# Kernel tuning notes

Hardware: AMD Instinct MI355X
Metric: run time of the kernel (lower is better)

## Reference

```python
import jax, jax.numpy as jnp
import numpy as np

CUTOFF = 5.0
N_GAUSS = 25
LOG2 = 0.6931471805599453
N_INTER = 3


def ssp(x):
    # shifted softplus used by SchNet
    return jax.nn.softplus(x) - LOG2


def setup_inputs() -> dict:
    key = jax.random.key(0)
    ks = jax.random.split(key, 16)
    B, A, N, F, G, Z = 16, 128, 127, 128, N_GAUSS, 100
    s = 1.0 / np.sqrt(F)
    emb = jax.random.normal(ks[0], (Z, F), jnp.float32)
    emb = emb.at[0].set(0.0)  # padding_idx=0
    inp = {
        "positions": jax.random.normal(ks[1], (B, A, 3), jnp.float32) * 3.0,
        "cell": jnp.zeros((B, 3, 3), jnp.float32),
        "cell_offset": jnp.zeros((B, A, N, 3), jnp.float32),
        "neighbor_mask": jnp.ones((B, A, N), jnp.float32),
        "embeddings": emb,
        "filt_W1": jax.random.normal(ks[2], (N_INTER, G, F), jnp.float32) / np.sqrt(G),
        "filt_b1": jnp.zeros((N_INTER, F), jnp.float32),
        "filt_W2": jax.random.normal(ks[3], (N_INTER, F, F), jnp.float32) * s,
        "filt_b2": jnp.zeros((N_INTER, F), jnp.float32),
        "in2f_W": jax.random.normal(ks[4], (N_INTER, F, F), jnp.float32) * s,
        "f2out_W": jax.random.normal(ks[5], (N_INTER, F, F), jnp.float32) * s,
        "f2out_b": jnp.zeros((N_INTER, F), jnp.float32),
        "dense_W": jax.random.normal(ks[6], (N_INTER, F, F), jnp.float32) * s,
        "dense_b": jnp.zeros((N_INTER, F), jnp.float32),
        "atomic_numbers": jax.random.randint(ks[7], (B, A), 1, Z).astype(jnp.int32),
        "neighbors": jax.random.randint(ks[8], (B, A, N), 0, A).astype(jnp.int32),
    }
    return inp


def _schnet_forward(positions, cell, cell_offset, neighbor_mask, embeddings,
                    filt_W1, filt_b1, filt_W2, filt_b2,
                    in2f_W, f2out_W, f2out_b, dense_W, dense_b,
                    atomic_numbers, neighbors):
    B, A, _ = positions.shape
    bidx = jnp.arange(B)[:, None, None]

    # ---- AtomDistances: gather neighbor positions, pairwise distances ----
    pos_nbh = positions[bidx, neighbors]            # [B,A,N,3]
    dvec = pos_nbh - positions[:, :, None, :]
    dvec = dvec + jnp.einsum('banj,bjc->banc', cell_offset, cell)
    d2 = jnp.sum(dvec * dvec, axis=-1)              # [B,A,N]
    m = neighbor_mask > 0
    r_ij = jnp.where(m, jnp.sqrt(jnp.where(m, d2, 1.0)), 0.0)

    # ---- GaussianSmearing(0, cutoff, 25) ----
    centers = jnp.linspace(0.0, CUTOFF, N_GAUSS, dtype=r_ij.dtype)
    width = centers[1] - centers[0]
    coeff = -0.5 / (width * width)
    diff = r_ij[..., None] - centers                # [B,A,N,G]
    f_ij = jnp.exp(coeff * diff * diff)

    # ---- CosineCutoff ----
    C = 0.5 * (jnp.cos(r_ij * jnp.pi / CUTOFF) + 1.0)
    C = C * (r_ij < CUTOFF).astype(r_ij.dtype)      # [B,A,N]

    # ---- embedding ----
    x = embeddings[atomic_numbers]                  # [B,A,F]

    # ---- interaction blocks (cfconv + dense residual) ----
    for l in range(N_INTER):
        W = ssp(jnp.einsum('bang,gf->banf', f_ij, filt_W1[l]) + filt_b1[l])
        W = jnp.einsum('banf,fg->bang', W, filt_W2[l]) + filt_b2[l]
        W = W * C[..., None]                        # [B,A,N,F]
        y = x @ in2f_W[l]                           # [B,A,F], no bias
        y_nbh = y[bidx, neighbors]                  # [B,A,N,F]
        agg = jnp.sum(y_nbh * W * neighbor_mask[..., None], axis=2)  # [B,A,F]
        v = ssp(agg @ f2out_W[l] + f2out_b[l])
        v = v @ dense_W[l] + dense_b[l]
        x = x + v
    return x


def reference(positions, cell, cell_offset, neighbor_mask, embeddings,
              filt_W1, filt_b1, filt_W2, filt_b2,
              in2f_W, f2out_W, f2out_b, dense_W, dense_b,
              atomic_numbers, neighbors):
    return _schnet_forward(positions, cell, cell_offset, neighbor_mask, embeddings,
                           filt_W1, filt_b1, filt_W2, filt_b2,
                           in2f_W, f2out_W, f2out_b, dense_W, dense_b,
                           atomic_numbers, neighbors)
```

## Files before the change

### kernel.cpp

```cpp
#include <hip/hip_runtime.h>
#include <math.h>

#define BB 16
#define AA 128
#define NNB 127
#define FF 128
#define GG 25

typedef __attribute__((ext_vector_type(8))) short bf16x8;
typedef __attribute__((ext_vector_type(4))) float f32x4;
typedef unsigned short ushort_t;

#define GLOBAL_LOAD_LDS16(gp, lp)                                                        \
    __builtin_amdgcn_global_load_lds((const __attribute__((address_space(1))) unsigned int*)(gp), \
                                     (__attribute__((address_space(3))) unsigned int*)(lp), 16, 0, 0)

__device__ __forceinline__ float ssp_f(float x) {
    return fmaxf(x, 0.f) + log1pf(__expf(-fabsf(x))) - 0.6931471805599453f;
}

__device__ __forceinline__ float ssp_fast(float x) {
    float e = __expf(-fabsf(x));
    float p = fmaf(e, 0.03215845f, -0.13606275f);
    p = fmaf(e, p, 0.28947478f);
    p = fmaf(e, p, -0.49190896f);
    p = fmaf(e, p, 0.99949556f);
    return fmaxf(x, 0.f) + e * p - 0.6931471805599453f;
}

__device__ __forceinline__ ushort_t f2bf(float f) {
    unsigned int u = __float_as_uint(f);
    unsigned int r = (u + 0x7fffu + ((u >> 16) & 1u)) >> 16;
    return (ushort_t)r;
}

__device__ __forceinline__ float bf2f(ushort_t h) {
    return __uint_as_float(((unsigned int)h) << 16);
}

__device__ __forceinline__ unsigned int pack2bf(float lo, float hi) {
    return (unsigned int)f2bf(lo) | ((unsigned int)f2bf(hi) << 16);
}

__global__ __launch_bounds__(256) void k_prep(const float* __restrict__ W1,
                                              const float* __restrict__ W2,
                                              const float* __restrict__ Win,
                                              const float* __restrict__ Wf,
                                              const float* __restrict__ Wd,
                                              ushort_t* __restrict__ w1t,
                                              ushort_t* __restrict__ w2s,
                                              ushort_t* __restrict__ whi,
                                              ushort_t* __restrict__ wlo) {
    int i = blockIdx.x * 256 + threadIdx.x;
    if (i < 3 * 128 * 32) {
        int l = i >> 12, rem = i & 4095, f = rem >> 5, g = rem & 31;
        float v = (g < GG) ? W1[l * GG * FF + g * FF + f] : 0.f;
        w1t[i] = f2bf(v);
    }
    if (i < 3 * 16384) {
        int l = i >> 14, rem = i & 16383, f = rem >> 7, k = rem & 127;
        w2s[l * 16384 + f * 128 + (k ^ ((f & 7) << 3))] = f2bf(W2[l * 16384 + k * FF + f]);
    }
    if (i < 9 * 16384) {
        int m = i / 49152;
        int rem = i - m * 49152;
        int l = rem >> 14;
        int rk = rem & 16383;
        int f = rk >> 7, k = rk & 127;
        const float* src = (m == 0) ? Win : ((m == 1) ? Wf : Wd);
        float v = src[l * 16384 + k * 128 + f];
        ushort_t h = f2bf(v);
        whi[i] = h;
        wlo[i] = f2bf(v - bf2f(h));
    }
}

__global__ __launch_bounds__(256) void k_init_x(const float* __restrict__ emb,
                                                const int* __restrict__ z,
                                                float* __restrict__ x) {
    int i = blockIdx.x * 256 + threadIdx.x;
    if (i < BB * AA * FF) {
        int row = i >> 7, f = i & 127;
        x[i] = emb[z[row] * FF + f];
    }
}

__global__ __launch_bounds__(512) void k_ffn(
    const float* __restrict__ agg, const float* __restrict__ x_in,
    float* __restrict__ x_out, float* __restrict__ y, float* __restrict__ out,
    const ushort_t* __restrict__ wfh, const ushort_t* __restrict__ wfl, const float* __restrict__ bfv_g,
    const ushort_t* __restrict__ wdh, const ushort_t* __restrict__ wdl, const float* __restrict__ bdv_g,
    const ushort_t* __restrict__ wih, const ushort_t* __restrict__ wil,
    int mode) {
    __shared__ ushort_t tsh[8][136];
    __shared__ ushort_t tsl[8][136];
    const int t = threadIdx.x;
    const int lane = t & 63, w = t >> 6;
    const int l15 = lane & 15, l4 = lane >> 4;
    const int r0 = blockIdx.x << 3;
    const int fcol = (w << 4) + l15;

    bf16x8 Ah[4], Al[4];

    auto loadA_global = [&](const float* __restrict__ M) {
#pragma unroll
        for (int ks = 0; ks < 4; ++ks) {
            float v[8];
            if (l15 < 8) {
                const float4* p = (const float4*)(M + ((size_t)(r0 + l15) << 7) + (ks << 5) + (l4 << 3));
                float4 a = p[0], b = p[1];
                v[0] = a.x; v[1] = a.y; v[2] = a.z; v[3] = a.w;
                v[4] = b.x; v[5] = b.y; v[6] = b.z; v[7] = b.w;
            } else {
#pragma unroll
                for (int j = 0; j < 8; ++j) v[j] = 0.f;
            }
#pragma unroll
            for (int j = 0; j < 8; ++j) {
                ushort_t h = f2bf(v[j]);
                Ah[ks][j] = (short)h;
                Al[ks][j] = (short)f2bf(v[j] - bf2f(h));
            }
        }
    };
    auto loadA_lds = [&]() {
#pragma unroll
        for (int ks = 0; ks < 4; ++ks) {
            if (l15 < 8) {
                const char* base = (const char*)&tsh[l15][0] + (ks << 6) + (l4 << 4);
                Ah[ks] = *(const bf16x8*)base;
                const char* basel = (const char*)&tsl[l15][0] + (ks << 6) + (l4 << 4);
                Al[ks] = *(const bf16x8*)basel;
            } else {
#pragma unroll
                for (int j = 0; j < 8; ++j) { Ah[ks][j] = 0; Al[ks][j] = 0; }
            }
        }
    };

    if (mode & 1) {
        loadA_global(agg);
        float bfv = bfv_g[fcol];
        f32x4 acc = {bfv, bfv, bfv, bfv};
#pragma unroll
        for (int ks = 0; ks < 4; ++ks) {
            const bf16x8 Bh = *(const bf16x8*)(wfh + ((size_t)fcol << 7) + (ks << 5) + (l4 << 3));
            const bf16x8 Bl = *(const bf16x8*)(wfl + ((size_t)fcol << 7) + (ks << 5) + (l4 << 3));
            acc = __builtin_amdgcn_mfma_f32_16x16x32_bf16(Al[ks], Bh, acc, 0, 0, 0);
            acc = __builtin_amdgcn_mfma_f32_16x16x32_bf16(Ah[ks], Bl, acc, 0, 0, 0);
            acc = __builtin_amdgcn_mfma_f32_16x16x32_bf16(Ah[ks], Bh, acc, 0, 0, 0);
        }
#pragma unroll
        for (int reg = 0; reg < 4; ++reg) {
            int r = (l4 << 2) + reg;
            if (r < 8) {
                float v = ssp_f(acc[reg]);
                ushort_t h = f2bf(v);
                tsh[r][fcol] = h;
                tsl[r][fcol] = f2bf(v - bf2f(h));
            }
        }
        __syncthreads();
        loadA_lds();
        float bdv = bdv_g[fcol];
        f32x4 acc2 = {bdv, bdv, bdv, bdv};
#pragma unroll
        for (int ks = 0; ks < 4; ++ks) {
            const bf16x8 Bh = *(const bf16x8*)(wdh + ((size_t)fcol << 7) + (ks << 5) + (l4 << 3));
            const bf16x8 Bl = *(const bf16x8*)(wdl + ((size_t)fcol << 7) + (ks << 5) + (l4 << 3));
            acc2 = __builtin_amdgcn_mfma_f32_16x16x32_bf16(Al[ks], Bh, acc2, 0, 0, 0);
            acc2 = __builtin_amdgcn_mfma_f32_16x16x32_bf16(Ah[ks], Bl, acc2, 0, 0, 0);
            acc2 = __builtin_amdgcn_mfma_f32_16x16x32_bf16(Ah[ks], Bh, acc2, 0, 0, 0);
        }
        __syncthreads();
#pragma unroll
        for (int reg = 0; reg < 4; ++reg) {
            int r = (l4 << 2) + reg;
            if (r < 8) {
                size_t gi = ((size_t)(r0 + r) << 7) + fcol;
                float xn = x_in[gi] + acc2[reg];
                x_out[gi] = xn;
                if (mode & 4) out[gi] = xn;
                if (mode & 2) {
                    ushort_t h = f2bf(xn);
                    tsh[r][fcol] = h;
                    tsl[r][fcol] = f2bf(xn - bf2f(h));
                }
            }
        }
        if (mode & 2) __syncthreads();
    }
    if (mode & 2) {
        if (mode & 1) loadA_lds(); else loadA_global(x_in);
        f32x4 acc3 = {0.f, 0.f, 0.f, 0.f};
#pragma unroll
        for (int ks = 0; ks < 4; ++ks) {
            const bf16x8 Bh = *(const bf16x8*)(wih + ((size_t)fcol << 7) + (ks << 5) + (l4 << 3));
            const bf16x8 Bl = *(const bf16x8*)(wil + ((size_t)fcol << 7) + (ks << 5) + (l4 << 3));
            acc3 = __builtin_amdgcn_mfma_f32_16x16x32_bf16(Al[ks], Bh, acc3, 0, 0, 0);
            acc3 = __builtin_amdgcn_mfma_f32_16x16x32_bf16(Ah[ks], Bl, acc3, 0, 0, 0);
            acc3 = __builtin_amdgcn_mfma_f32_16x16x32_bf16(Ah[ks], Bh, acc3, 0, 0, 0);
        }
#pragma unroll
        for (int reg = 0; reg < 4; ++reg) {
            int r = (l4 << 2) + reg;
            if (r < 8) y[((size_t)(r0 + r) << 7) + fcol] = acc3[reg];
        }
    }
}

#define SMEM_BYTES 67072

__global__ __launch_bounds__(512, 4) void k_cfconv(
    const float* __restrict__ positions, const float* __restrict__ cell,
    const float* __restrict__ cell_offset, const float* __restrict__ nmask,
    const int* __restrict__ neighbors,
    const ushort_t* __restrict__ w1t, const float* __restrict__ b1,
    const ushort_t* __restrict__ w2s, const float* __restrict__ b2,
    const float* __restrict__ y, float* __restrict__ agg) {
    extern __shared__ char smem[];
    float* cm_s = (float*)(smem + 65536);
    int* nbr_s = (int*)(smem + 66048);
    float* r_s = (float*)(smem + 66560);
    float* y_s = (float*)smem;
    float* red_s = (float*)smem;

    const int row = blockIdx.x;
    const int b = row >> 7;
    const int t = threadIdx.x;
    const int lane = t & 63, w = t >> 6;
    const int l15 = lane & 15, l4 = lane >> 4;

    {
        const char* gsrc = (const char*)w2s;
#pragma unroll
        for (int i = 0; i < 4; ++i) {
            int blk = (w << 2) + i;
            GLOBAL_LOAD_LDS16(gsrc + (blk << 10) + (lane << 4), smem + 32768 + (blk << 10));
        }
    }

    if (t < NNB) {
        int nb = neighbors[row * NNB + t];
        nbr_s[t] = nb;
        float px = positions[row * 3 + 0], py = positions[row * 3 + 1], pz = positions[row * 3 + 2];
        int nrow = b * AA + nb;
        float qx = positions[nrow * 3 + 0], qy = positions[nrow * 3 + 1], qz = positions[nrow * 3 + 2];
        const float* co = cell_offset + (size_t)row * NNB * 3 + (size_t)t * 3;
        const float* cl = cell + b * 9;
        float c0 = co[0], c1 = co[1], c2 = co[2];
        float ox = c0 * cl[0] + c1 * cl[3] + c2 * cl[6];
        float oy = c0 * cl[1] + c1 * cl[4] + c2 * cl[7];
        float oz = c0 * cl[2] + c1 * cl[5] + c2 * cl[8];
        float dx = qx - px + ox, dy = qy - py + oy, dz = qz - pz + oz;
        float d2 = dx * dx + dy * dy + dz * dz;
        float mk = nmask[row * NNB + t];
        float r = (mk > 0.f) ? sqrtf(d2) : 0.f;
        r_s[t] = r;
        float Cc = 0.5f * (__cosf(r * (3.14159265358979323846f / 5.0f)) + 1.f);
        Cc = (r < 5.0f) ? Cc : 0.f;
        cm_s[t] = Cc * mk;
    } else if (t == NNB) {
        cm_s[NNB] = 0.f; nbr_s[NNB] = 0; r_s[NNB] = 1e9f;
    }
    __syncthreads();

    {
        const int nrow = (w << 4) + l15;
        const float rv = r_s[nrow];
        const float width = 5.0f / (GG - 1);
        const float coeff = -0.5f / (width * width);
        bf16x8 fb;
#pragma unroll
        for (int j = 0; j < 8; ++j) {
            int g = (l4 << 3) + j;
            float d = rv - g * width;
            float v = (g < GG && nrow < NNB) ? __expf(coeff * d * d) : 0.f;
            fb[j] = (short)f2bf(v);
        }
        const int base = nrow * 256;
        const int sw = (nrow & 7) << 4;
#pragma unroll
        for (int ft = 0; ft < 8; ++ft) {
            bf16x8 aw = *(const bf16x8*)(w1t + ((ft << 4) + l15) * 32 + (l4 << 3));
            const int f0 = (ft << 4) + (l4 << 2);
            f32x4 c0 = *(const f32x4*)(b1 + f0);
            f32x4 d = __builtin_amdgcn_mfma_f32_16x16x32_bf16(aw, fb, c0, 0, 0, 0);
            unsigned long long pk =
                (unsigned long long)pack2bf(ssp_fast(d[0]), ssp_fast(d[1])) |
                ((unsigned long long)pack2bf(ssp_fast(d[2]), ssp_fast(d[3])) << 32);
            *(unsigned long long*)(smem + base + ((f0 << 1) ^ sw)) = pk;
        }
    }
    __syncthreads();

    const int wr = w >> 2, wc = w & 3;
    f32x4 acc[4][2];
#pragma unroll
    for (int mi = 0; mi < 4; ++mi)
#pragma unroll
        for (int ft = 0; ft < 2; ++ft) {
            float b2v = b2[(wc << 5) + (ft << 4) + l15];
            f32x4 c0 = {b2v, b2v, b2v, b2v};
            acc[mi][ft] = c0;
        }
#pragma unroll
    for (int ks = 0; ks < 4; ++ks) {
        bf16x8 ha[4];
#pragma unroll
        for (int mi = 0; mi < 4; ++mi) {
            int n = (wr << 6) + (mi << 4) + l15;
            ha[mi] = *(const bf16x8*)(smem + n * 256 + ((((ks << 2) + l4) << 4) ^ ((n & 7) << 4)));
        }
        bf16x8 wbv[2];
#pragma unroll
        for (int ft = 0; ft < 2; ++ft) {
            int f = (wc << 5) + (ft << 4) + l15;
            wbv[ft] = *(const bf16x8*)(smem + 32768 + f * 256 + ((((ks << 2) + l4) << 4) ^ ((f & 7) << 4)));
        }
#pragma unroll
        for (int mi = 0; mi < 4; ++mi) {
            acc[mi][0] = __builtin_amdgcn_mfma_f32_16x16x32_bf16(ha[mi], wbv[0], acc[mi][0], 0, 0, 0);
            acc[mi][1] = __builtin_amdgcn_mfma_f32_16x16x32_bf16(ha[mi], wbv[1], acc[mi][1], 0, 0, 0);
        }
    }
    __syncthreads();

    {
        const int bA = b * AA;
#pragma unroll
        for (int ii = 0; ii < 8; ++ii) {
            int c = t + (ii << 9);
            int n = c >> 5, sub = c & 31;
            int nb = nbr_s[n];
            int e0 = (sub << 2) ^ ((n & 7) << 2);
            const float* gp = y + (((size_t)(bA + nb)) << 7) + e0;
            GLOBAL_LOAD_LDS16(gp, smem + ((size_t)c << 4));
        }
    }
    __syncthreads();

    float part[2] = {0.f, 0.f};
#pragma unroll
    for (int mi = 0; mi < 4; ++mi) {
#pragma unroll
        for (int r = 0; r < 4; ++r) {
            int n = (wr << 6) + (mi << 4) + (l4 << 2) + r;
            if (n < NNB) {
                float cmv = cm_s[n];
                const float* yrow = y_s + (n << 7);
                int sx = (n & 7) << 2;
                part[0] = fmaf(yrow[((wc << 5) + l15) ^ sx], acc[mi][0][r] * cmv, part[0]);
                part[1] = fmaf(yrow[((wc << 5) + 16 + l15) ^ sx], acc[mi][1][r] * cmv, part[1]);
            }
        }
    }
    __syncthreads();
    {
        int xg = l4 << 3;
        red_s[(w << 7) + (l4 << 5) + (l15 ^ xg)] = part[0];
        red_s[(w << 7) + (l4 << 5) + ((16 + l15) ^ xg)] = part[1];
    }
    __syncthreads();
    if (t < FF) {
        int wcf = t >> 5, fl = t & 31;
        float s = 0.f;
#pragma unroll
        for (int wr2 = 0; wr2 < 2; ++wr2)
#pragma unroll
            for (int g = 0; g < 4; ++g)
                s += red_s[(((wr2 << 2) + wcf) << 7) + (g << 5) + (fl ^ (g << 3))];
        agg[(size_t)row * FF + t] = s;
    }
}

extern "C" void kernel_launch(void* const* d_in, const int* in_sizes, int n_in,
                              void* d_out, int out_size, void* d_ws, size_t ws_size,
                              hipStream_t stream) {
    const float* positions   = (const float*)d_in[0];
    const float* cell        = (const float*)d_in[1];
    const float* cell_offset = (const float*)d_in[2];
    const float* nmask       = (const float*)d_in[3];
    const float* emb         = (const float*)d_in[4];
    const float* filt_W1     = (const float*)d_in[5];
    const float* filt_b1     = (const float*)d_in[6];
    const float* filt_W2     = (const float*)d_in[7];
    const float* filt_b2     = (const float*)d_in[8];
    const float* in2f_W      = (const float*)d_in[9];
    const float* f2out_W     = (const float*)d_in[10];
    const float* f2out_b     = (const float*)d_in[11];
    const float* dense_W     = (const float*)d_in[12];
    const float* dense_b     = (const float*)d_in[13];
    const int* atomic_numbers = (const int*)d_in[14];
    const int* neighbors      = (const int*)d_in[15];
    float* out = (float*)d_out;

    float* x   = (float*)d_ws;
    float* yb  = x + BB * AA * FF;
    float* agg = yb + BB * AA * FF;
    ushort_t* w1t = (ushort_t*)(agg + BB * AA * FF);
    ushort_t* w2s = w1t + 3 * 128 * 32;
    ushort_t* whi = w2s + 3 * 16384;
    ushort_t* wlo = whi + 9 * 16384;

    k_prep<<<576, 256, 0, stream>>>(filt_W1, filt_W2, in2f_W, f2out_W, dense_W,
                                    w1t, w2s, whi, wlo);
    k_init_x<<<(BB * AA * FF + 255) / 256, 256, 0, stream>>>(emb, atomic_numbers, x);

    k_ffn<<<256, 512, 0, stream>>>(x, x, x, yb, out,
                                   whi + 3 * 16384, wlo + 3 * 16384, f2out_b,
                                   whi + 6 * 16384, wlo + 6 * 16384, dense_b,
                                   whi + 0 * 16384, wlo + 0 * 16384,
                                   2);
    for (int l = 0; l < 3; ++l) {
        k_cfconv<<<BB * AA, 512, SMEM_BYTES, stream>>>(
            positions, cell, cell_offset, nmask, neighbors,
            w1t + (size_t)l * 128 * 32, filt_b1 + (size_t)l * FF,
            w2s + (size_t)l * 128 * 128, filt_b2 + (size_t)l * FF,
            yb, agg);
        int nextl = (l < 2) ? (l + 1) : 0;
        int mode = 1 | ((l < 2) ? 2 : 0) | ((l == 2) ? 4 : 0);
        k_ffn<<<256, 512, 0, stream>>>(agg, x, x, yb, out,
                                       whi + (3 + l) * 16384, wlo + (3 + l) * 16384, f2out_b + (size_t)l * FF,
                                       whi + (6 + l) * 16384, wlo + (6 + l) * 16384, dense_b + (size_t)l * FF,
                                       whi + nextl * 16384, wlo + nextl * 16384,
                                       mode);
    }
}
```

Before: 153.9 us.

## Load W2 fragments from global into registers and gather y directly, halving LDS

The cfconv kernel no longer stages the filter W2 matrix or the gathered neighbor y rows in LDS. W2 is prepacked into MFMA fragment order so each lane loads its B operand straight from global memory, with the next k-slice prefetched one step ahead. Neighbor y values are read directly from global in the accumulation loop, which drops one barrier and one LDS staging pass. LDS use falls from about 67KB to 34KB, and launch bounds rise to 6 blocks per CU for more occupancy, at the cost of more scattered global and L2 traffic and more register pressure.

After: 127.5 us. -17.2%, faster.

```diff
diff --git a/kernel.cpp b/kernel.cpp
--- a/kernel.cpp
+++ b/kernel.cpp
@@ -10,10 +10,6 @@
 typedef __attribute__((ext_vector_type(8))) short bf16x8;
 typedef __attribute__((ext_vector_type(4))) float f32x4;
 typedef unsigned short ushort_t;
-
-#define GLOBAL_LOAD_LDS16(gp, lp)                                                        \
-    __builtin_amdgcn_global_load_lds((const __attribute__((address_space(1))) unsigned int*)(gp), \
-                                     (__attribute__((address_space(3))) unsigned int*)(lp), 16, 0, 0)
 
 __device__ __forceinline__ float ssp_f(float x) {
     return fmaxf(x, 0.f) + log1pf(__expf(-fabsf(x))) - 0.6931471805599453f;
@@ -48,7 +44,7 @@
                                               const float* __restrict__ Wf,
                                               const float* __restrict__ Wd,
                                               ushort_t* __restrict__ w1t,
-                                              ushort_t* __restrict__ w2s,
+                                              ushort_t* __restrict__ w2f,
                                               ushort_t* __restrict__ whi,
                                               ushort_t* __restrict__ wlo) {
     int i = blockIdx.x * 256 + threadIdx.x;
@@ -58,8 +54,13 @@
         w1t[i] = f2bf(v);
     }
     if (i < 3 * 16384) {
-        int l = i >> 14, rem = i & 16383, f = rem >> 7, k = rem & 127;
-        w2s[l * 16384 + f * 128 + (k ^ ((f & 7) << 3))] = f2bf(W2[l * 16384 + k * FF + f]);
+        int l = i >> 14, e = i & 16383;
+        int u = e >> 3, j = e & 7;
+        int ks = u >> 9, rem = u & 511;
+        int wcft = rem >> 6, lane = rem & 63;
+        int f = (wcft >> 1) * 32 + (wcft & 1) * 16 + (lane & 15);
+        int k = ks * 32 + (lane >> 4) * 8 + j;
+        w2f[i] = f2bf(W2[l * 16384 + k * 128 + f]);
     }
     if (i < 9 * 16384) {
         int m = i / 49152;
@@ -209,20 +210,19 @@
     }
 }
 
-#define SMEM_BYTES 67072
-
-__global__ __launch_bounds__(512, 4) void k_cfconv(
+#define SMEM_BYTES 34304
+
+__global__ __launch_bounds__(512, 6) void k_cfconv(
     const float* __restrict__ positions, const float* __restrict__ cell,
     const float* __restrict__ cell_offset, const float* __restrict__ nmask,
     const int* __restrict__ neighbors,
     const ushort_t* __restrict__ w1t, const float* __restrict__ b1,
-    const ushort_t* __restrict__ w2s, const float* __restrict__ b2,
+    const ushort_t* __restrict__ w2f, const float* __restrict__ b2,
     const float* __restrict__ y, float* __restrict__ agg) {
     extern __shared__ char smem[];
-    float* cm_s = (float*)(smem + 65536);
-    int* nbr_s = (int*)(smem + 66048);
-    float* r_s = (float*)(smem + 66560);
-    float* y_s = (float*)smem;
+    float* cm_s = (float*)(smem + 32768);
+    int* nbr_s = (int*)(smem + 33280);
+    float* r_s = (float*)(smem + 33792);
     float* red_s = (float*)smem;
 
     const int row = blockIdx.x;
@@ -230,15 +230,7 @@
     const int t = threadIdx.x;
     const int lane = t & 63, w = t >> 6;
     const int l15 = lane & 15, l4 = lane >> 4;
-
-    {
-        const char* gsrc = (const char*)w2s;
-#pragma unroll
-        for (int i = 0; i < 4; ++i) {
-            int blk = (w << 2) + i;
-            GLOBAL_LOAD_LDS16(gsrc + (blk << 10) + (lane << 4), smem + 32768 + (blk << 10));
-        }
-    }
+    const int wr = w >> 2, wc = w & 3;
 
     if (t < NNB) {
         int nb = neighbors[row * NNB + t];
@@ -292,9 +284,11 @@
             *(unsigned long long*)(smem + base + ((f0 << 1) ^ sw)) = pk;
         }
     }
+
+#define W2LD(ks, ft) (*(const bf16x8*)(w2f + (((((ks) << 3) + (wc << 1) + (ft)) << 6) + lane) * 8))
+    bf16x8 wb0 = W2LD(0, 0), wb1 = W2LD(0, 1);
     __syncthreads();
 
-    const int wr = w >> 2, wc = w & 3;
     f32x4 acc[4][2];
 #pragma unroll
     for (int mi = 0; mi < 4; ++mi)
@@ -306,60 +300,48 @@
         }
 #pragma unroll
     for (int ks = 0; ks < 4; ++ks) {
+        bf16x8 wn0, wn1;
+        if (ks < 3) { wn0 = W2LD(ks + 1, 0); wn1 = W2LD(ks + 1, 1); }
         bf16x8 ha[4];
 #pragma unroll
         for (int mi = 0; mi < 4; ++mi) {
             int n = (wr << 6) + (mi << 4) + l15;
             ha[mi] = *(const bf16x8*)(smem + n * 256 + ((((ks << 2) + l4) << 4) ^ ((n & 7) << 4)));
         }
-        bf16x8 wbv[2];
-#pragma unroll
-        for (int ft = 0; ft < 2; ++ft) {
-            int f = (wc << 5) + (ft << 4) + l15;
-            wbv[ft] = *(const bf16x8*)(smem + 32768 + f * 256 + ((((ks << 2) + l4) << 4) ^ ((f & 7) << 4)));
-        }
 #pragma unroll
         for (int mi = 0; mi < 4; ++mi) {
-            acc[mi][0] = __builtin_amdgcn_mfma_f32_16x16x32_bf16(ha[mi], wbv[0], acc[mi][0], 0, 0, 0);
-            acc[mi][1] = __builtin_amdgcn_mfma_f32_16x16x32_bf16(ha[mi], wbv[1], acc[mi][1], 0, 0, 0);
-        }
-    }
+            acc[mi][0] = __builtin_amdgcn_mfma_f32_16x16x32_bf16(ha[mi], wb0, acc[mi][0], 0, 0, 0);
+            acc[mi][1] = __builtin_amdgcn_mfma_f32_16x16x32_bf16(ha[mi], wb1, acc[mi][1], 0, 0, 0);
+        }
+        if (ks < 3) { wb0 = wn0; wb1 = wn1; }
+    }
+#undef W2LD
     __syncthreads();
 
-    {
-        const int bA = b * AA;
-#pragma unroll
-        for (int ii = 0; ii < 8; ++ii) {
-            int c = t + (ii << 9);
-            int n = c >> 5, sub = c & 31;
-            int nb = nbr_s[n];
-            int e0 = (sub << 2) ^ ((n & 7) << 2);
-            const float* gp = y + (((size_t)(bA + nb)) << 7) + e0;
-            GLOBAL_LOAD_LDS16(gp, smem + ((size_t)c << 4));
-        }
-    }
-    __syncthreads();
-
-    float part[2] = {0.f, 0.f};
+    float part0 = 0.f, part1 = 0.f;
+    const float* ybase = y + ((size_t)(b * AA) << 7) + (wc << 5) + l15;
 #pragma unroll
     for (int mi = 0; mi < 4; ++mi) {
+        float yv0[4], yv1[4], cmv[4];
 #pragma unroll
         for (int r = 0; r < 4; ++r) {
             int n = (wr << 6) + (mi << 4) + (l4 << 2) + r;
-            if (n < NNB) {
-                float cmv = cm_s[n];
-                const float* yrow = y_s + (n << 7);
-                int sx = (n & 7) << 2;
-                part[0] = fmaf(yrow[((wc << 5) + l15) ^ sx], acc[mi][0][r] * cmv, part[0]);
-                part[1] = fmaf(yrow[((wc << 5) + 16 + l15) ^ sx], acc[mi][1][r] * cmv, part[1]);
-            }
-        }
-    }
-    __syncthreads();
+            int nb = nbr_s[n];
+            cmv[r] = cm_s[n];
+            const float* yr = ybase + ((size_t)nb << 7);
+            yv0[r] = yr[0];
+            yv1[r] = yr[16];
+        }
+#pragma unroll
+        for (int r = 0; r < 4; ++r) {
+            part0 = fmaf(yv0[r], acc[mi][0][r] * cmv[r], part0);
+            part1 = fmaf(yv1[r], acc[mi][1][r] * cmv[r], part1);
+        }
+    }
     {
         int xg = l4 << 3;
-        red_s[(w << 7) + (l4 << 5) + (l15 ^ xg)] = part[0];
-        red_s[(w << 7) + (l4 << 5) + ((16 + l15) ^ xg)] = part[1];
+        red_s[(w << 7) + (l4 << 5) + (l15 ^ xg)] = part0;
+        red_s[(w << 7) + (l4 << 5) + ((16 + l15) ^ xg)] = part1;
     }
     __syncthreads();
     if (t < FF) {
@@ -399,12 +381,12 @@
     float* yb  = x + BB * AA * FF;
     float* agg = yb + BB * AA * FF;
     ushort_t* w1t = (ushort_t*)(agg + BB * AA * FF);
-    ushort_t* w2s = w1t + 3 * 128 * 32;
-    ushort_t* whi = w2s + 3 * 16384;
+    ushort_t* w2f = w1t + 3 * 128 * 32;
+    ushort_t* whi = w2f + 3 * 16384;
     ushort_t* wlo = whi + 9 * 16384;
 
     k_prep<<<576, 256, 0, stream>>>(filt_W1, filt_W2, in2f_W, f2out_W, dense_W,
-                                    w1t, w2s, whi, wlo);
+                                    w1t, w2f, whi, wlo);
     k_init_x<<<(BB * AA * FF + 255) / 256, 256, 0, stream>>>(emb, atomic_numbers, x);
 
     k_ffn<<<256, 512, 0, stream>>>(x, x, x, yb, out,
@@ -416,7 +398,7 @@
         k_cfconv<<<BB * AA, 512, SMEM_BYTES, stream>>>(
             positions, cell, cell_offset, nmask, neighbors,
             w1t + (size_t)l * 128 * 32, filt_b1 + (size_t)l * FF,
-            w2s + (size_t)l * 128 * 128, filt_b2 + (size_t)l * FF,
+            w2f + (size_t)l * 16384, filt_b2 + (size_t)l * FF,
             yb, agg);
         int nextl = (l < 2) ? (l + 1) : 0;
         int mode = 1 | ((l < 2) ? 2 : 0) | ((l == 2) ? 4 : 0);
```
